# Optimization experiments

Measured on AMD Instinct MI355X. Metric: run time of the kernel, lower is better.

Reference implementation:

```python
import jax, jax.numpy as jnp
import numpy as np

H = 256; W = 256; N = 512
TANFOVX = 0.5; TANFOVY = 0.5
FX = W / (2.0 * TANFOVX)   # focal_x
FY = H / (2.0 * TANFOVY)   # focal_y


def _quat_to_rot(q):
    # q: [N,4] (w,x,y,z), normalized inside
    q = q / jnp.linalg.norm(q, axis=-1, keepdims=True)
    r, x, y, z = q[:, 0], q[:, 1], q[:, 2], q[:, 3]
    R = jnp.stack([
        1 - 2 * (y * y + z * z), 2 * (x * y - r * z), 2 * (x * z + r * y),
        2 * (x * y + r * z), 1 - 2 * (x * x + z * z), 2 * (y * z - r * x),
        2 * (x * z - r * y), 2 * (y * z + r * x), 1 - 2 * (x * x + y * y)],
        axis=-1).reshape(-1, 3, 3)
    return R


def _camera():
    # row-vector convention: t = [p,1] @ V ; full proj = V @ Pclip (3DGS style)
    V = np.eye(4, dtype=np.float32)
    V[3, :3] = [0.0, 0.0, 5.0]            # camera 5 units back along -z
    zn, zf = 0.01, 100.0
    P = np.zeros((4, 4), np.float32)
    P[0, 0] = 1.0 / TANFOVX
    P[1, 1] = 1.0 / TANFOVY
    P[2, 2] = zf / (zf - zn)
    P[3, 2] = -zf * zn / (zf - zn)
    P[2, 3] = 1.0
    return jnp.asarray(V), jnp.asarray(V @ P)


def setup_inputs() -> dict:
    key = jax.random.key(0)
    ks = jax.random.split(key, 5)
    means3D = jax.random.normal(ks[0], (N, 3), jnp.float32)
    opacities = jax.random.uniform(ks[1], (N, 1), jnp.float32)
    colors_precomp = jax.random.uniform(ks[2], (N, 3), jnp.float32)
    scales = 0.05 * jax.random.uniform(ks[3], (N, 3), jnp.float32) + 0.01
    rotations = jax.random.normal(ks[4], (N, 4), jnp.float32)
    viewmatrix, projmatrix = _camera()
    return dict(means3D=means3D, opacities=opacities,
                colors_precomp=colors_precomp, scales=scales,
                rotations=rotations, bg=jnp.zeros((3,), jnp.float32),
                viewmatrix=viewmatrix, projmatrix=projmatrix,
                campos=jnp.array([0.0, 0.0, -5.0], jnp.float32))


def _rasterize(means3D, opacities, colors, scales, rotations, bg,
               viewmatrix, projmatrix):
    n = means3D.shape[0]
    # --- 3D covariance: Sigma = (R S)(R S)^T ---
    Rm = _quat_to_rot(rotations)
    M = Rm * scales[:, None, :]                       # [N,3,3]
    Sigma = jnp.einsum('nij,nkj->nik', M, M)
    # --- camera-space positions ---
    ph = jnp.concatenate([means3D, jnp.ones((n, 1), means3D.dtype)], axis=1)
    t = ph @ viewmatrix                               # [N,4]
    tz = t[:, 2]
    tzc = jnp.maximum(tz, 1e-4)
    limx, limy = 1.3 * TANFOVX, 1.3 * TANFOVY
    txc = jnp.clip(t[:, 0] / tzc, -limx, limx) * tzc
    tyc = jnp.clip(t[:, 1] / tzc, -limy, limy) * tzc
    # --- EWA 2D covariance ---
    z0 = jnp.zeros_like(tz)
    J = jnp.stack([
        jnp.stack([FX / tzc, z0, -FX * txc / (tzc * tzc)], axis=-1),
        jnp.stack([z0, FY / tzc, -FY * tyc / (tzc * tzc)], axis=-1)],
        axis=1)                                        # [N,2,3]
    Wc = viewmatrix[:3, :3].T                          # column-vector rotation
    T = jnp.einsum('nij,jk->nik', J, Wc)               # [N,2,3]
    cov2d = jnp.einsum('nij,njk,nlk->nil', T, Sigma, T)
    cov2d = cov2d + 0.3 * jnp.eye(2, dtype=cov2d.dtype)  # low-pass dilation
    c00, c01, c11 = cov2d[:, 0, 0], cov2d[:, 0, 1], cov2d[:, 1, 1]
    det = c00 * c11 - c01 * c01
    det_inv = 1.0 / jnp.where(det != 0, det, 1.0)
    A = c11 * det_inv; B = -c01 * det_inv; C = c00 * det_inv  # conic
    mid = 0.5 * (c00 + c11)
    lam = mid + jnp.sqrt(jnp.maximum(mid * mid - det, 0.1))
    visible = (det > 0) & (tz > 0.2)
    radii = jnp.where(visible, jnp.ceil(3.0 * jnp.sqrt(lam)), 0.0).astype(jnp.int32)
    # --- screen-space means (ndc2pix) ---
    phom = ph @ projmatrix
    pw = 1.0 / (phom[:, 3] + 1e-7)
    mx = ((phom[:, 0] * pw + 1.0) * W - 1.0) * 0.5
    my = ((phom[:, 1] * pw + 1.0) * H - 1.0) * 0.5
    # --- depth sort (front-to-back) ---
    order = jnp.argsort(tz)
    mx, my = mx[order], my[order]
    A_, B_, C_ = A[order], B[order], C[order]
    op = opacities[order, 0]
    vis = visible[order]
    cols = colors[order]
    zs = tz[order]
    # --- per-pixel Gaussian evaluation [P, N] ---
    xs = jnp.arange(W, dtype=means3D.dtype)
    ys = jnp.arange(H, dtype=means3D.dtype)
    pix_x = jnp.tile(xs, H)
    pix_y = jnp.repeat(ys, W)
    dx = mx[None, :] - pix_x[:, None]
    dy = my[None, :] - pix_y[:, None]
    power = -0.5 * (A_[None, :] * dx * dx + C_[None, :] * dy * dy) \
            - B_[None, :] * dx * dy
    alpha = jnp.minimum(0.99, op[None, :] * jnp.exp(power))
    valid = (power <= 0.0) & vis[None, :] & (alpha >= 1.0 / 255.0)
    alpha = jnp.where(valid, alpha, 0.0)
    # --- front-to-back alpha compositing ---
    cum = jnp.cumprod(1.0 - alpha, axis=1)
    Tprev = jnp.concatenate(
        [jnp.ones((alpha.shape[0], 1), alpha.dtype), cum[:, :-1]], axis=1)
    wgt = alpha * Tprev                               # [P,N]
    Tfinal = cum[:, -1]
    color = wgt @ cols + Tfinal[:, None] * bg[None, :]
    depth = wgt @ zs
    color = color.reshape(H, W, 3).transpose(2, 0, 1)  # [3,H,W]
    return color, depth.reshape(H, W), Tfinal.reshape(H, W), radii


def reference(means3D, opacities, colors_precomp, scales, rotations, bg,
              viewmatrix, projmatrix, campos):
    return _rasterize(means3D, opacities, colors_precomp, scales, rotations,
                      bg, viewmatrix, projmatrix)
```

## Files before the change

kernel.cpp:

```cpp
#include <hip/hip_runtime.h>
#include <hip/hip_fp16.h>
#include <math.h>

#define NG 512
#define WI 256
#define HI 256
#define FXc 256.0f
#define FYc 256.0f
#define P2MIN -7.9943534368588578f

#if __has_builtin(__builtin_amdgcn_exp2f)
#define EXP2F(x) __builtin_amdgcn_exp2f(x)
#else
#define EXP2F(x) exp2f(x)
#endif

__global__ __launch_bounds__(512) void gs_prep_sort(
    const float* __restrict__ means,
    const float* __restrict__ opac,
    const float* __restrict__ cols,
    const float* __restrict__ scales,
    const float* __restrict__ rots,
    const float* __restrict__ Vm,
    const float* __restrict__ Pm,
    float* __restrict__ ws_s,
    float2* __restrict__ ws_cull,
    float* __restrict__ radii_out)
{
    __shared__ __align__(16) float key[NG];
    int g = threadIdx.x;

    float qr = rots[g*4+0], qx = rots[g*4+1], qy = rots[g*4+2], qz = rots[g*4+3];
    float inv = rsqrtf(qr*qr + qx*qx + qy*qy + qz*qz);
    qr *= inv; qx *= inv; qy *= inv; qz *= inv;
    float R00 = 1.f - 2.f*(qy*qy + qz*qz);
    float R01 = 2.f*(qx*qy - qr*qz);
    float R02 = 2.f*(qx*qz + qr*qy);
    float R10 = 2.f*(qx*qy + qr*qz);
    float R11 = 1.f - 2.f*(qx*qx + qz*qz);
    float R12 = 2.f*(qy*qz - qr*qx);
    float R20 = 2.f*(qx*qz - qr*qy);
    float R21 = 2.f*(qy*qz + qr*qx);
    float R22 = 1.f - 2.f*(qx*qx + qy*qy);

    float s0 = scales[g*3+0], s1 = scales[g*3+1], s2 = scales[g*3+2];
    float M00=R00*s0, M01=R01*s1, M02=R02*s2;
    float M10=R10*s0, M11=R11*s1, M12=R12*s2;
    float M20=R20*s0, M21=R21*s1, M22=R22*s2;

    float S00 = M00*M00 + M01*M01 + M02*M02;
    float S01 = M00*M10 + M01*M11 + M02*M12;
    float S02 = M00*M20 + M01*M21 + M02*M22;
    float S11 = M10*M10 + M11*M11 + M12*M12;
    float S12 = M10*M20 + M11*M21 + M12*M22;
    float S22 = M20*M20 + M21*M21 + M22*M22;

    float px = means[g*3+0], py = means[g*3+1], pz = means[g*3+2];
    float t0 = px*Vm[0] + py*Vm[4] + pz*Vm[8]  + Vm[12];
    float t1 = px*Vm[1] + py*Vm[5] + pz*Vm[9]  + Vm[13];
    float tz = px*Vm[2] + py*Vm[6] + pz*Vm[10] + Vm[14];
    float tzc = fmaxf(tz, 1e-4f);
    const float limx = 1.3f*0.5f, limy = 1.3f*0.5f;
    float txc = fminf(fmaxf(t0 / tzc, -limx), limx) * tzc;
    float tyc = fminf(fmaxf(t1 / tzc, -limy), limy) * tzc;

    float J00 = FXc / tzc;
    float J02 = -FXc * txc / (tzc * tzc);
    float J11 = FYc / tzc;
    float J12 = -FYc * tyc / (tzc * tzc);

    float Ta0 = J00*Vm[0] + J02*Vm[2];
    float Ta1 = J00*Vm[4] + J02*Vm[6];
    float Ta2 = J00*Vm[8] + J02*Vm[10];
    float Tb0 = J11*Vm[1] + J12*Vm[2];
    float Tb1 = J11*Vm[5] + J12*Vm[6];
    float Tb2 = J11*Vm[9] + J12*Vm[10];

    float u0 = Ta0*S00 + Ta1*S01 + Ta2*S02;
    float u1 = Ta0*S01 + Ta1*S11 + Ta2*S12;
    float u2 = Ta0*S02 + Ta1*S12 + Ta2*S22;
    float v0 = Tb0*S00 + Tb1*S01 + Tb2*S02;
    float v1 = Tb0*S01 + Tb1*S11 + Tb2*S12;
    float v2 = Tb0*S02 + Tb1*S12 + Tb2*S22;
    float c00 = u0*Ta0 + u1*Ta1 + u2*Ta2 + 0.3f;
    float c01 = u0*Tb0 + u1*Tb1 + u2*Tb2;
    float c11 = v0*Tb0 + v1*Tb1 + v2*Tb2 + 0.3f;

    float det = c00*c11 - c01*c01;
    float det_inv = 1.f / ((det != 0.f) ? det : 1.f);
    float Aa =  c11 * det_inv;
    float Bb = -c01 * det_inv;
    float Cc =  c00 * det_inv;

    float mid = 0.5f*(c00 + c11);
    float lam = mid + sqrtf(fmaxf(mid*mid - det, 0.1f));
    bool vis = (det > 0.f) && (tz > 0.2f);
    int rad = vis ? (int)ceilf(3.f*sqrtf(lam)) : 0;
    radii_out[g] = (float)rad;

    float h0 = px*Pm[0] + py*Pm[4] + pz*Pm[8]  + Pm[12];
    float h1 = px*Pm[1] + py*Pm[5] + pz*Pm[9]  + Pm[13];
    float h3 = px*Pm[3] + py*Pm[7] + pz*Pm[11] + Pm[15];
    float pw = 1.f / (h3 + 1e-7f);
    float mx = ((h0*pw + 1.f)*WI - 1.f)*0.5f;
    float my = ((h1*pw + 1.f)*HI - 1.f)*0.5f;

    float opv = vis ? opac[g] : 0.f;

    const float L2E = 1.4426950408889634f;
    float A2 = -0.5f*L2E*Aa;
    float B2 = -L2E*Bb;
    float C2 = -0.5f*L2E*Cc;
    float lop = (opv > 0.f) ? log2f(opv) : -3.0e38f;

    float a  = 0.5f*L2E*Aa;
    float c  = 0.5f*L2E*Cc;
    float b  = L2E*Bb;
    float qmax  = lop + 7.9943534368588578f;
    float cmarg = c - b*b/(4.f*a);
    float amarg = a - b*b/(4.f*c);
    float dxmin = fmaxf(0.f, fmaxf(-mx, mx - 255.f));
    bool alive = vis && (opv > 0.f) && (qmax >= 0.f) && (cmarg > 0.f)
                 && (amarg*dxmin*dxmin <= qmax);
    float ycull = alive ? sqrtf(qmax/cmarg) + 0.0625f : -1.f;

    union { __half2 h; float f; } prg, pbt;
    prg.h = __halves2half2(__float2half_rn(cols[g*3+0]), __float2half_rn(cols[g*3+1]));
    pbt.h = __halves2half2(__float2half_rn(cols[g*3+2]), __float2half_rn(tz));

    key[g] = tz;
    __syncthreads();

    float k = key[g];
    int rank = 0;
    const float4* k4 = (const float4*)key;
    #pragma unroll 4
    for (int j = 0; j < NG/4; ++j) {
        float4 kk = k4[j];
        int j4 = j*4;
        rank += (kk.x < k) || ((kk.x == k) && (j4+0 < g));
        rank += (kk.y < k) || ((kk.y == k) && (j4+1 < g));
        rank += (kk.z < k) || ((kk.z == k) && (j4+2 < g));
        rank += (kk.w < k) || ((kk.w == k) && (j4+3 < g));
    }

    float4* dst = (float4*)(ws_s + rank*8);
    dst[0] = make_float4(mx, my, A2, B2);
    dst[1] = make_float4(C2, lop, prg.f, pbt.f);
    ws_cull[rank] = make_float2(my, ycull);
}

__global__ __launch_bounds__(256) void gs_raster(
    const float4* __restrict__ gsr,
    const float4* __restrict__ cullp,
    const float* __restrict__ bg,
    float* __restrict__ out)
{
    __shared__ __align__(16) float4 cs[NG*2];
    __shared__ int wtot[4];

    int tx   = threadIdx.x;
    int lane = tx & 63;
    int wv   = tx >> 6;
    int y    = blockIdx.x;
    float yf = (float)y;

    float4 cp = cullp[tx];
    bool f0 = fabsf(cp.x - yf) <= cp.y;
    bool f1 = fabsf(cp.z - yf) <= cp.w;

    unsigned long long m0 = __ballot(f0);
    unsigned long long m1 = __ballot(f1);
    unsigned long long lt = (lane == 63) ? 0x7fffffffffffffffULL : ((1ULL << lane) - 1ULL);
    lt = (1ULL << lane) - 1ULL;
    int pre = __popcll(m0 & lt) + __popcll(m1 & lt);
    if (lane == 0) wtot[wv] = __popcll(m0) + __popcll(m1);
    __syncthreads();

    int base = 0, n = 0;
    #pragma unroll
    for (int w2 = 0; w2 < 4; ++w2) {
        int t = wtot[w2];
        base += (w2 < wv) ? t : 0;
        n += t;
    }

    int p0 = base + pre;
    if (f0) {
        cs[p0*2+0] = gsr[tx*4+0];
        cs[p0*2+1] = gsr[tx*4+1];
    }
    if (f1) {
        int p1 = p0 + (f0 ? 1 : 0);
        cs[p1*2+0] = gsr[tx*4+2];
        cs[p1*2+1] = gsr[tx*4+3];
    }
    __syncthreads();

    float pxf = (float)tx;
    float T = 1.f, cr = 0.f, cg = 0.f, cb = 0.f, dp = 0.f;
    for (int j = 0; j < n; ++j) {
        float4 q0 = cs[2*j+0];
        float4 q1 = cs[2*j+1];
        float dx = q0.x - pxf;
        float dy = q0.y - yf;
        float lop = q1.y;
        float p2 = fmaf(q0.z, dx*dx, fmaf(q1.x, dy*dy, fmaf(q0.w, dx*dy, lop)));
        float al = fminf(0.99f, EXP2F(p2));
        al = ((p2 <= lop) && (p2 >= P2MIN)) ? al : 0.f;
        float w = al * T;
        union { float f; __half2 h; } urg, ubt;
        urg.f = q1.z; ubt.f = q1.w;
        cr = fmaf(w, __low2float(urg.h),  cr);
        cg = fmaf(w, __high2float(urg.h), cg);
        cb = fmaf(w, __low2float(ubt.h),  cb);
        dp = fmaf(w, __high2float(ubt.h), dp);
        T -= w;
    }

    const int HW = WI * HI;
    int p = y * WI + tx;
    out[p]        = cr + T * bg[0];
    out[HW+p]     = cg + T * bg[1];
    out[2*HW+p]   = cb + T * bg[2];
    out[3*HW+p]   = dp;
    out[4*HW+p]   = T;
}

extern "C" void kernel_launch(void* const* d_in, const int* in_sizes, int n_in,
                              void* d_out, int out_size, void* d_ws, size_t ws_size,
                              hipStream_t stream)
{
    const float* means  = (const float*)d_in[0];
    const float* opac   = (const float*)d_in[1];
    const float* cols   = (const float*)d_in[2];
    const float* scales = (const float*)d_in[3];
    const float* rots   = (const float*)d_in[4];
    const float* bg     = (const float*)d_in[5];
    const float* Vm     = (const float*)d_in[6];
    const float* Pm     = (const float*)d_in[7];

    float* out  = (float*)d_out;
    float* ws_s = (float*)d_ws;
    float2* ws_cull = (float2*)(ws_s + 8*NG);
    float* radii_out = out + 5*WI*HI;

    hipLaunchKernelGGL(gs_prep_sort, dim3(1), dim3(NG), 0, stream,
                       means, opac, cols, scales, rots, Vm, Pm, ws_s, ws_cull, radii_out);
    hipLaunchKernelGGL(gs_raster, dim3(HI), dim3(WI), 0, stream,
                       (const float4*)ws_s, (const float4*)ws_cull, bg, out);
}
```

Measured before the change: 90.39 us.

## Fuse preprocessing and depth sort into per-row raster kernel

Merges the single-block preprocessing/sort kernel into the raster kernel. Each of the 256 row blocks now recomputes all 512 Gaussians' projection, culls them by row, and ranks only the surviving ones by depth in shared memory. It also folds the dy-dependent terms into per-row coefficients, so the inner loop needs fewer FMAs. This removes a kernel launch, the serial one-block prep stage and the workspace round trip, at the cost of redundant per-block preprocessing and an O(n^2) rank over the culled set.

```diff
diff --git a/kernel.cpp b/kernel.cpp
--- a/kernel.cpp
+++ b/kernel.cpp
@@ -15,7 +15,7 @@
 #define EXP2F(x) exp2f(x)
 #endif
 
-__global__ __launch_bounds__(512) void gs_prep_sort(
+__global__ __launch_bounds__(256) void gs_fused(
     const float* __restrict__ means,
     const float* __restrict__ opac,
     const float* __restrict__ cols,
@@ -23,140 +23,12 @@
     const float* __restrict__ rots,
     const float* __restrict__ Vm,
     const float* __restrict__ Pm,
-    float* __restrict__ ws_s,
-    float2* __restrict__ ws_cull,
-    float* __restrict__ radii_out)
-{
-    __shared__ __align__(16) float key[NG];
-    int g = threadIdx.x;
-
-    float qr = rots[g*4+0], qx = rots[g*4+1], qy = rots[g*4+2], qz = rots[g*4+3];
-    float inv = rsqrtf(qr*qr + qx*qx + qy*qy + qz*qz);
-    qr *= inv; qx *= inv; qy *= inv; qz *= inv;
-    float R00 = 1.f - 2.f*(qy*qy + qz*qz);
-    float R01 = 2.f*(qx*qy - qr*qz);
-    float R02 = 2.f*(qx*qz + qr*qy);
-    float R10 = 2.f*(qx*qy + qr*qz);
-    float R11 = 1.f - 2.f*(qx*qx + qz*qz);
-    float R12 = 2.f*(qy*qz - qr*qx);
-    float R20 = 2.f*(qx*qz - qr*qy);
-    float R21 = 2.f*(qy*qz + qr*qx);
-    float R22 = 1.f - 2.f*(qx*qx + qy*qy);
-
-    float s0 = scales[g*3+0], s1 = scales[g*3+1], s2 = scales[g*3+2];
-    float M00=R00*s0, M01=R01*s1, M02=R02*s2;
-    float M10=R10*s0, M11=R11*s1, M12=R12*s2;
-    float M20=R20*s0, M21=R21*s1, M22=R22*s2;
-
-    float S00 = M00*M00 + M01*M01 + M02*M02;
-    float S01 = M00*M10 + M01*M11 + M02*M12;
-    float S02 = M00*M20 + M01*M21 + M02*M22;
-    float S11 = M10*M10 + M11*M11 + M12*M12;
-    float S12 = M10*M20 + M11*M21 + M12*M22;
-    float S22 = M20*M20 + M21*M21 + M22*M22;
-
-    float px = means[g*3+0], py = means[g*3+1], pz = means[g*3+2];
-    float t0 = px*Vm[0] + py*Vm[4] + pz*Vm[8]  + Vm[12];
-    float t1 = px*Vm[1] + py*Vm[5] + pz*Vm[9]  + Vm[13];
-    float tz = px*Vm[2] + py*Vm[6] + pz*Vm[10] + Vm[14];
-    float tzc = fmaxf(tz, 1e-4f);
-    const float limx = 1.3f*0.5f, limy = 1.3f*0.5f;
-    float txc = fminf(fmaxf(t0 / tzc, -limx), limx) * tzc;
-    float tyc = fminf(fmaxf(t1 / tzc, -limy), limy) * tzc;
-
-    float J00 = FXc / tzc;
-    float J02 = -FXc * txc / (tzc * tzc);
-    float J11 = FYc / tzc;
-    float J12 = -FYc * tyc / (tzc * tzc);
-
-    float Ta0 = J00*Vm[0] + J02*Vm[2];
-    float Ta1 = J00*Vm[4] + J02*Vm[6];
-    float Ta2 = J00*Vm[8] + J02*Vm[10];
-    float Tb0 = J11*Vm[1] + J12*Vm[2];
-    float Tb1 = J11*Vm[5] + J12*Vm[6];
-    float Tb2 = J11*Vm[9] + J12*Vm[10];
-
-    float u0 = Ta0*S00 + Ta1*S01 + Ta2*S02;
-    float u1 = Ta0*S01 + Ta1*S11 + Ta2*S12;
-    float u2 = Ta0*S02 + Ta1*S12 + Ta2*S22;
-    float v0 = Tb0*S00 + Tb1*S01 + Tb2*S02;
-    float v1 = Tb0*S01 + Tb1*S11 + Tb2*S12;
-    float v2 = Tb0*S02 + Tb1*S12 + Tb2*S22;
-    float c00 = u0*Ta0 + u1*Ta1 + u2*Ta2 + 0.3f;
-    float c01 = u0*Tb0 + u1*Tb1 + u2*Tb2;
-    float c11 = v0*Tb0 + v1*Tb1 + v2*Tb2 + 0.3f;
-
-    float det = c00*c11 - c01*c01;
-    float det_inv = 1.f / ((det != 0.f) ? det : 1.f);
-    float Aa =  c11 * det_inv;
-    float Bb = -c01 * det_inv;
-    float Cc =  c00 * det_inv;
-
-    float mid = 0.5f*(c00 + c11);
-    float lam = mid + sqrtf(fmaxf(mid*mid - det, 0.1f));
-    bool vis = (det > 0.f) && (tz > 0.2f);
-    int rad = vis ? (int)ceilf(3.f*sqrtf(lam)) : 0;
-    radii_out[g] = (float)rad;
-
-    float h0 = px*Pm[0] + py*Pm[4] + pz*Pm[8]  + Pm[12];
-    float h1 = px*Pm[1] + py*Pm[5] + pz*Pm[9]  + Pm[13];
-    float h3 = px*Pm[3] + py*Pm[7] + pz*Pm[11] + Pm[15];
-    float pw = 1.f / (h3 + 1e-7f);
-    float mx = ((h0*pw + 1.f)*WI - 1.f)*0.5f;
-    float my = ((h1*pw + 1.f)*HI - 1.f)*0.5f;
-
-    float opv = vis ? opac[g] : 0.f;
-
-    const float L2E = 1.4426950408889634f;
-    float A2 = -0.5f*L2E*Aa;
-    float B2 = -L2E*Bb;
-    float C2 = -0.5f*L2E*Cc;
-    float lop = (opv > 0.f) ? log2f(opv) : -3.0e38f;
-
-    float a  = 0.5f*L2E*Aa;
-    float c  = 0.5f*L2E*Cc;
-    float b  = L2E*Bb;
-    float qmax  = lop + 7.9943534368588578f;
-    float cmarg = c - b*b/(4.f*a);
-    float amarg = a - b*b/(4.f*c);
-    float dxmin = fmaxf(0.f, fmaxf(-mx, mx - 255.f));
-    bool alive = vis && (opv > 0.f) && (qmax >= 0.f) && (cmarg > 0.f)
-                 && (amarg*dxmin*dxmin <= qmax);
-    float ycull = alive ? sqrtf(qmax/cmarg) + 0.0625f : -1.f;
-
-    union { __half2 h; float f; } prg, pbt;
-    prg.h = __halves2half2(__float2half_rn(cols[g*3+0]), __float2half_rn(cols[g*3+1]));
-    pbt.h = __halves2half2(__float2half_rn(cols[g*3+2]), __float2half_rn(tz));
-
-    key[g] = tz;
-    __syncthreads();
-
-    float k = key[g];
-    int rank = 0;
-    const float4* k4 = (const float4*)key;
-    #pragma unroll 4
-    for (int j = 0; j < NG/4; ++j) {
-        float4 kk = k4[j];
-        int j4 = j*4;
-        rank += (kk.x < k) || ((kk.x == k) && (j4+0 < g));
-        rank += (kk.y < k) || ((kk.y == k) && (j4+1 < g));
-        rank += (kk.z < k) || ((kk.z == k) && (j4+2 < g));
-        rank += (kk.w < k) || ((kk.w == k) && (j4+3 < g));
-    }
-
-    float4* dst = (float4*)(ws_s + rank*8);
-    dst[0] = make_float4(mx, my, A2, B2);
-    dst[1] = make_float4(C2, lop, prg.f, pbt.f);
-    ws_cull[rank] = make_float2(my, ycull);
-}
-
-__global__ __launch_bounds__(256) void gs_raster(
-    const float4* __restrict__ gsr,
-    const float4* __restrict__ cullp,
     const float* __restrict__ bg,
     float* __restrict__ out)
 {
+    __shared__ __align__(16) float4 us[NG*2];
     __shared__ __align__(16) float4 cs[NG*2];
+    __shared__ float skey[NG];
     __shared__ int wtot[4];
 
     int tx   = threadIdx.x;
@@ -165,14 +37,128 @@
     int y    = blockIdx.x;
     float yf = (float)y;
 
-    float4 cp = cullp[tx];
-    bool f0 = fabsf(cp.x - yf) <= cp.y;
-    bool f1 = fabsf(cp.z - yf) <= cp.w;
+    float4 q0r[2], q1r[2];
+    float tzs[2], myv[2], ycl[2], radf[2];
+
+    #pragma unroll
+    for (int i = 0; i < 2; ++i) {
+        int g = 2*tx + i;
+
+        float qr = rots[g*4+0], qx = rots[g*4+1], qy = rots[g*4+2], qz = rots[g*4+3];
+        float inv = rsqrtf(qr*qr + qx*qx + qy*qy + qz*qz);
+        qr *= inv; qx *= inv; qy *= inv; qz *= inv;
+        float R00 = 1.f - 2.f*(qy*qy + qz*qz);
+        float R01 = 2.f*(qx*qy - qr*qz);
+        float R02 = 2.f*(qx*qz + qr*qy);
+        float R10 = 2.f*(qx*qy + qr*qz);
+        float R11 = 1.f - 2.f*(qx*qx + qz*qz);
+        float R12 = 2.f*(qy*qz - qr*qx);
+        float R20 = 2.f*(qx*qz - qr*qy);
+        float R21 = 2.f*(qy*qz + qr*qx);
+        float R22 = 1.f - 2.f*(qx*qx + qy*qy);
+
+        float s0 = scales[g*3+0], s1 = scales[g*3+1], s2 = scales[g*3+2];
+        float M00=R00*s0, M01=R01*s1, M02=R02*s2;
+        float M10=R10*s0, M11=R11*s1, M12=R12*s2;
+        float M20=R20*s0, M21=R21*s1, M22=R22*s2;
+
+        float S00 = M00*M00 + M01*M01 + M02*M02;
+        float S01 = M00*M10 + M01*M11 + M02*M12;
+        float S02 = M00*M20 + M01*M21 + M02*M22;
+        float S11 = M10*M10 + M11*M11 + M12*M12;
+        float S12 = M10*M20 + M11*M21 + M12*M22;
+        float S22 = M20*M20 + M21*M21 + M22*M22;
+
+        float px = means[g*3+0], py = means[g*3+1], pz = means[g*3+2];
+        float t0 = px*Vm[0] + py*Vm[4] + pz*Vm[8]  + Vm[12];
+        float t1 = px*Vm[1] + py*Vm[5] + pz*Vm[9]  + Vm[13];
+        float tz = px*Vm[2] + py*Vm[6] + pz*Vm[10] + Vm[14];
+        float tzc = fmaxf(tz, 1e-4f);
+        const float limx = 1.3f*0.5f, limy = 1.3f*0.5f;
+        float txc = fminf(fmaxf(t0 / tzc, -limx), limx) * tzc;
+        float tyc = fminf(fmaxf(t1 / tzc, -limy), limy) * tzc;
+
+        float J00 = FXc / tzc;
+        float J02 = -FXc * txc / (tzc * tzc);
+        float J11 = FYc / tzc;
+        float J12 = -FYc * tyc / (tzc * tzc);
+
+        float Ta0 = J00*Vm[0] + J02*Vm[2];
+        float Ta1 = J00*Vm[4] + J02*Vm[6];
+        float Ta2 = J00*Vm[8] + J02*Vm[10];
+        float Tb0 = J11*Vm[1] + J12*Vm[2];
+        float Tb1 = J11*Vm[5] + J12*Vm[6];
+        float Tb2 = J11*Vm[9] + J12*Vm[10];
+
+        float u0 = Ta0*S00 + Ta1*S01 + Ta2*S02;
+        float u1 = Ta0*S01 + Ta1*S11 + Ta2*S12;
+        float u2 = Ta0*S02 + Ta1*S12 + Ta2*S22;
+        float v0 = Tb0*S00 + Tb1*S01 + Tb2*S02;
+        float v1 = Tb0*S01 + Tb1*S11 + Tb2*S12;
+        float v2 = Tb0*S02 + Tb1*S12 + Tb2*S22;
+        float c00 = u0*Ta0 + u1*Ta1 + u2*Ta2 + 0.3f;
+        float c01 = u0*Tb0 + u1*Tb1 + u2*Tb2;
+        float c11 = v0*Tb0 + v1*Tb1 + v2*Tb2 + 0.3f;
+
+        float det = c00*c11 - c01*c01;
+        float det_inv = 1.f / ((det != 0.f) ? det : 1.f);
+        float Aa =  c11 * det_inv;
+        float Bb = -c01 * det_inv;
+        float Cc =  c00 * det_inv;
+
+        float mid = 0.5f*(c00 + c11);
+        float lam = mid + sqrtf(fmaxf(mid*mid - det, 0.1f));
+        bool vis = (det > 0.f) && (tz > 0.2f);
+        radf[i] = vis ? ceilf(3.f*sqrtf(lam)) : 0.f;
+
+        float h0 = px*Pm[0] + py*Pm[4] + pz*Pm[8]  + Pm[12];
+        float h1 = px*Pm[1] + py*Pm[5] + pz*Pm[9]  + Pm[13];
+        float h3 = px*Pm[3] + py*Pm[7] + pz*Pm[11] + Pm[15];
+        float pw = 1.f / (h3 + 1e-7f);
+        float mx = ((h0*pw + 1.f)*WI - 1.f)*0.5f;
+        float my = ((h1*pw + 1.f)*HI - 1.f)*0.5f;
+
+        float opv = vis ? opac[g] : 0.f;
+
+        const float L2E = 1.4426950408889634f;
+        float A2 = -0.5f*L2E*Aa;
+        float B2 = -L2E*Bb;
+        float C2 = -0.5f*L2E*Cc;
+        float lop = (opv > 0.f) ? log2f(opv) : -3.0e38f;
+
+        float a  = 0.5f*L2E*Aa;
+        float c  = 0.5f*L2E*Cc;
+        float b  = L2E*Bb;
+        float qmax  = lop + 7.9943534368588578f;
+        float cmarg = c - b*b/(4.f*a);
+        float amarg = a - b*b/(4.f*c);
+        float dxmin = fmaxf(0.f, fmaxf(-mx, mx - 255.f));
+        bool alive = vis && (opv > 0.f) && (qmax >= 0.f) && (cmarg > 0.f)
+                     && (amarg*dxmin*dxmin <= qmax);
+        ycl[i] = alive ? sqrtf(qmax/cmarg) + 0.0625f : -1.f;
+
+        union { __half2 h; float f; } prg, pbt;
+        prg.h = __halves2half2(__float2half_rn(cols[g*3+0]), __float2half_rn(cols[g*3+1]));
+        pbt.h = __halves2half2(__float2half_rn(cols[g*3+2]), __float2half_rn(tz));
+
+        q0r[i] = make_float4(mx, my, A2, B2);
+        q1r[i] = make_float4(C2, lop, prg.f, pbt.f);
+        tzs[i] = tz;
+        myv[i] = my;
+    }
+
+    if (y == 0) {
+        float* radii_out = out + 5*WI*HI;
+        radii_out[2*tx]   = radf[0];
+        radii_out[2*tx+1] = radf[1];
+    }
+
+    bool f0 = fabsf(myv[0] - yf) <= ycl[0];
+    bool f1 = fabsf(myv[1] - yf) <= ycl[1];
 
     unsigned long long m0 = __ballot(f0);
     unsigned long long m1 = __ballot(f1);
-    unsigned long long lt = (lane == 63) ? 0x7fffffffffffffffULL : ((1ULL << lane) - 1ULL);
-    lt = (1ULL << lane) - 1ULL;
+    unsigned long long lt = (1ULL << lane) - 1ULL;
     int pre = __popcll(m0 & lt) + __popcll(m1 & lt);
     if (lane == 0) wtot[wv] = __popcll(m0) + __popcll(m1);
     __syncthreads();
@@ -187,30 +173,47 @@
 
     int p0 = base + pre;
     if (f0) {
-        cs[p0*2+0] = gsr[tx*4+0];
-        cs[p0*2+1] = gsr[tx*4+1];
+        us[p0*2+0] = q0r[0];
+        us[p0*2+1] = q1r[0];
+        skey[p0]   = tzs[0];
     }
     if (f1) {
         int p1 = p0 + (f0 ? 1 : 0);
-        cs[p1*2+0] = gsr[tx*4+2];
-        cs[p1*2+1] = gsr[tx*4+3];
+        us[p1*2+0] = q0r[1];
+        us[p1*2+1] = q1r[1];
+        skey[p1]   = tzs[1];
+    }
+    __syncthreads();
+
+    if (tx < n) {
+        float k = skey[tx];
+        int rank = 0;
+        for (int j = 0; j < n; ++j) {
+            float o = skey[j];
+            rank += (o < k) || ((o == k) && (j < tx));
+        }
+        float4 a = us[2*tx+0];
+        float4 b = us[2*tx+1];
+        float dy = a.y - yf;
+        float c1 = a.w * dy;
+        float c0 = fmaf(b.x*dy, dy, b.y);
+        cs[2*rank+0] = make_float4(a.x, a.z, c1, c0);
+        cs[2*rank+1] = make_float4(b.y, b.z, b.w, 0.f);
     }
     __syncthreads();
 
     float pxf = (float)tx;
     float T = 1.f, cr = 0.f, cg = 0.f, cb = 0.f, dp = 0.f;
     for (int j = 0; j < n; ++j) {
-        float4 q0 = cs[2*j+0];
-        float4 q1 = cs[2*j+1];
-        float dx = q0.x - pxf;
-        float dy = q0.y - yf;
-        float lop = q1.y;
-        float p2 = fmaf(q0.z, dx*dx, fmaf(q1.x, dy*dy, fmaf(q0.w, dx*dy, lop)));
+        float4 a = cs[2*j+0];
+        float4 b = cs[2*j+1];
+        float dx = a.x - pxf;
+        float p2 = fmaf(fmaf(a.y, dx, a.z), dx, a.w);
         float al = fminf(0.99f, EXP2F(p2));
-        al = ((p2 <= lop) && (p2 >= P2MIN)) ? al : 0.f;
+        al = ((p2 <= b.x) && (p2 >= P2MIN)) ? al : 0.f;
         float w = al * T;
         union { float f; __half2 h; } urg, ubt;
-        urg.f = q1.z; ubt.f = q1.w;
+        urg.f = b.y; ubt.f = b.z;
         cr = fmaf(w, __low2float(urg.h),  cr);
         cg = fmaf(w, __high2float(urg.h), cg);
         cb = fmaf(w, __low2float(ubt.h),  cb);
@@ -240,13 +243,8 @@
     const float* Vm     = (const float*)d_in[6];
     const float* Pm     = (const float*)d_in[7];
 
-    float* out  = (float*)d_out;
-    float* ws_s = (float*)d_ws;
-    float2* ws_cull = (float2*)(ws_s + 8*NG);
-    float* radii_out = out + 5*WI*HI;
-
-    hipLaunchKernelGGL(gs_prep_sort, dim3(1), dim3(NG), 0, stream,
-                       means, opac, cols, scales, rots, Vm, Pm, ws_s, ws_cull, radii_out);
-    hipLaunchKernelGGL(gs_raster, dim3(HI), dim3(WI), 0, stream,
-                       (const float4*)ws_s, (const float4*)ws_cull, bg, out);
+    float* out = (float*)d_out;
+
+    hipLaunchKernelGGL(gs_fused, dim3(HI), dim3(WI), 0, stream,
+                       means, opac, cols, scales, rots, Vm, Pm, bg, out);
 }
```

New measurement: 77.15 us. -14.6%, faster.
